# Performance work log

Measured on AMD Instinct MI355X. Metric: run time of the kernel, lower is better.

## Reference

```python
import jax, jax.numpy as jnp
import numpy as np

B, S, E, H = 2, 2048, 2048, 16
D = E // H          # head_dim = 128
RD = 128            # rotary_emb_dim (== head_dim here)
BASE = 10000.0


def setup_inputs() -> dict:
    key = jax.random.key(0)
    k1, k2, k3, k4, k5 = jax.random.split(key, 5)
    scale = 0.02
    return {
        "x": jax.random.normal(k1, (B, S, E), dtype=jnp.float32),
        "wqkv_w": jax.random.normal(k2, (3 * E, E), dtype=jnp.float32) * scale,
        "wqkv_b": jax.random.normal(k3, (3 * E,), dtype=jnp.float32) * scale,
        "out_w": jax.random.normal(k4, (E, E), dtype=jnp.float32) * scale,
        "out_b": jax.random.normal(k5, (E,), dtype=jnp.float32) * scale,
    }


def _rope_cos_sin(seqlen, dtype):
    inv_freq = 1.0 / (BASE ** (jnp.arange(0, RD, 2, dtype=jnp.float32) / RD))
    t = jnp.arange(seqlen, dtype=jnp.float32)
    freqs = jnp.outer(t, inv_freq)          # (S, RD//2)
    return jnp.cos(freqs).astype(dtype), jnp.sin(freqs).astype(dtype)


def _apply_rotary(v, cos, sin):
    # v: (B, S, H, D); rotate first RD dims (here RD == D)
    v_rot, v_pass = v[..., :RD], v[..., RD:]
    v1, v2 = jnp.split(v_rot, 2, axis=-1)    # each (B, S, H, RD//2)
    c = cos[None, :, None, :]
    s = sin[None, :, None, :]
    rot = jnp.concatenate([v1 * c - v2 * s, v1 * s + v2 * c], axis=-1)
    return jnp.concatenate([rot, v_pass], axis=-1)


def reference(x, wqkv_w, wqkv_b, out_w, out_b):
    b, s, e = x.shape
    # column-parallel QKV projection (world size 1)
    qkv = jnp.einsum("bse,fe->bsf", x, wqkv_w) + wqkv_b     # (B, S, 3E)
    qkv = qkv.reshape(b, s, 3, H, D)
    cos, sin = _rope_cos_sin(s, x.dtype)
    q = _apply_rotary(qkv[:, :, 0], cos, sin)               # (B, S, H, D)
    k = _apply_rotary(qkv[:, :, 1], cos, sin)
    v = qkv[:, :, 2]
    # causal self-attention, softmax_scale = 1/sqrt(head_dim)
    scale = 1.0 / jnp.sqrt(jnp.asarray(D, dtype=x.dtype))
    scores = jnp.einsum("bshd,bthd->bhst", q, k) * scale    # (B, H, S, S)
    causal_mask = jnp.tril(jnp.ones((s, s), dtype=bool))
    scores = jnp.where(causal_mask[None, None], scores, jnp.finfo(x.dtype).min)
    probs = jax.nn.softmax(scores, axis=-1)
    ctx = jnp.einsum("bhst,bthd->bshd", probs, v)           # (B, S, H, D)
    # row-parallel output projection
    out = jnp.einsum("bse,fe->bsf", ctx.reshape(b, s, e), out_w) + out_b
    return out
```

## Files before the change

### kernel.cpp

```cpp
#include <hip/hip_runtime.h>
#include <cstdint>
#include <cstddef>

#define Bd 2
#define Sd 2048
#define Ed 2048
#define Hd 16
#define Dd 128
#define N3E 6144
#define ATT_SCALE 0.08838834764831845f

typedef short bf16x8 __attribute__((ext_vector_type(8)));
typedef float f32x4 __attribute__((ext_vector_type(4)));

__device__ __forceinline__ float bf2f(unsigned short u) {
    union { unsigned int u; float f; } c;
    c.u = ((unsigned int)u) << 16;
    return c.f;
}
__device__ __forceinline__ unsigned short f2bf(float f) {
    union { float f; unsigned int u; } c;
    c.f = f;
    unsigned int x = c.u;
    x += 0x7FFFu + ((x >> 16) & 1u);
    return (unsigned short)(x >> 16);
}

__device__ __forceinline__ void gl2lds16(const void* g, void* l) {
    __builtin_amdgcn_global_load_lds(
        (const __attribute__((address_space(1))) void*)g,
        (__attribute__((address_space(3))) void*)l, 16, 0, 0);
}

__global__ void cvt_f32_bf16(const float* __restrict__ src,
                             unsigned short* __restrict__ dst, int n) {
    int i = (blockIdx.x * 256 + threadIdx.x) * 4;
    if (i >= n) return;
    const float4 v = *(const float4*)(src + i);
    dst[i + 0] = f2bf(v.x);
    dst[i + 1] = f2bf(v.y);
    dst[i + 2] = f2bf(v.z);
    dst[i + 3] = f2bf(v.w);
}

template <int MODE>
__global__ void gemm_bt(const unsigned short* __restrict__ A,
                        const unsigned short* __restrict__ Bm,
                        const float* __restrict__ bias,
                        void* __restrict__ o0, void* __restrict__ o1,
                        void* __restrict__ o2, int Ndim, int K) {
    __shared__ __align__(16) unsigned short As[128 * 64];
    __shared__ __align__(16) unsigned short Bs[128 * 64];

    const int tid = threadIdx.x;
    const int lane = tid & 63;
    const int wave = tid >> 6;
    const int quad = lane >> 4;
    const int l16 = lane & 15;
    const int wr = wave >> 1;
    const int wc = wave & 1;

    const int n0 = blockIdx.x * 128;
    const int m0 = blockIdx.y * 128;

    const unsigned short* Ab = A + (size_t)m0 * K;
    const unsigned short* Bb = Bm + (size_t)n0 * K;

    const f32x4 fzero = {0.f, 0.f, 0.f, 0.f};
    f32x4 acc[4][4];
#pragma unroll
    for (int i = 0; i < 4; i++)
#pragma unroll
        for (int j = 0; j < 4; j++) acc[i][j] = fzero;

    for (int k0 = 0; k0 < K; k0 += 64) {
        __syncthreads();
#pragma unroll
        for (int it = 0; it < 4; ++it) {
            int L = it * 256 + tid;
            int row = L >> 3;
            int cs = L & 7;
            int gc = cs ^ (row & 7);
            gl2lds16(Ab + row * K + k0 + gc * 8, (void*)(As + L * 8));
            gl2lds16(Bb + row * K + k0 + gc * 8, (void*)(Bs + L * 8));
        }
        __syncthreads();
#pragma unroll
        for (int kk = 0; kk < 2; ++kk) {
            bf16x8 af[4], bfr[4];
#pragma unroll
            for (int i = 0; i < 4; i++) {
                int row = wr * 64 + i * 16 + l16;
                int cs = kk * 4 + quad;
                af[i] = *(const bf16x8*)(As + row * 64 + (cs ^ (row & 7)) * 8);
            }
#pragma unroll
            for (int j = 0; j < 4; j++) {
                int row = wc * 64 + j * 16 + l16;
                int cs = kk * 4 + quad;
                bfr[j] = *(const bf16x8*)(Bs + row * 64 + (cs ^ (row & 7)) * 8);
            }
#pragma unroll
            for (int i = 0; i < 4; i++)
#pragma unroll
                for (int j = 0; j < 4; j++)
                    acc[i][j] = __builtin_amdgcn_mfma_f32_16x16x32_bf16(
                        af[i], bfr[j], acc[i][j], 0, 0, 0);
        }
    }

#pragma unroll
    for (int j = 0; j < 4; j++) {
        int col = n0 + wc * 64 + j * 16 + l16;
        float bv = bias[col];
#pragma unroll
        for (int i = 0; i < 4; i++) {
            int rbase = m0 + wr * 64 + i * 16 + quad * 4;
#pragma unroll
            for (int r = 0; r < 4; r++) {
                float val = acc[i][j][r] + bv;
                int row = rbase + r;
                if (MODE == 0) {
                    ((float*)o0)[(size_t)row * Ndim + col] = val;
                } else {
                    int b = row >> 11;
                    int s = row & 2047;
                    int c = col >> 11;
                    int h = (col >> 7) & 15;
                    int d = col & 127;
                    unsigned short* dst = (c == 0) ? (unsigned short*)o0
                                        : (c == 1) ? (unsigned short*)o1
                                                   : (unsigned short*)o2;
                    dst[((size_t)(b * Hd + h) * Sd + s) * Dd + d] = f2bf(val);
                }
            }
        }
    }
}

__global__ void rope_qk(unsigned short* __restrict__ q,
                        unsigned short* __restrict__ k) {
    int idx = blockIdx.x * 256 + threadIdx.x;
    const int half = Bd * Hd * Sd * 64;
    unsigned short* p = (idx < half) ? q : k;
    int i = (idx < half) ? idx : idx - half;
    int j = i & 63;
    int s = (i >> 6) & (Sd - 1);
    int bh = i >> 17;
    int base = (bh * Sd + s) * Dd;
    float inv_freq = __expf(-(float)j * (9.210340371976184f / 64.0f));
    float fr = (float)s * inv_freq;
    float sn, cs;
    __sincosf(fr, &sn, &cs);
    float v1 = bf2f(p[base + j]);
    float v2 = bf2f(p[base + j + 64]);
    p[base + j] = f2bf(v1 * cs - v2 * sn);
    p[base + j + 64] = f2bf(v1 * sn + v2 * cs);
}

__global__ void transpose_v(const unsigned short* __restrict__ v,
                            unsigned short* __restrict__ vt) {
    __shared__ unsigned short t[32][33];
    int bh = blockIdx.z;
    int s0 = blockIdx.x * 32;
    int d0 = blockIdx.y * 32;
    int tx = threadIdx.x, ty = threadIdx.y;
    const unsigned short* src = v + ((size_t)bh * Sd + s0) * Dd + d0;
    for (int r = ty; r < 32; r += 8) t[r][tx] = src[(size_t)r * Dd + tx];
    __syncthreads();
    unsigned short* dst = vt + ((size_t)bh * Dd + d0) * Sd + s0;
    for (int r = ty; r < 32; r += 8) dst[(size_t)r * Sd + tx] = t[tx][r];
}

__global__ __launch_bounds__(256, 4) void flash_attn(
    const unsigned short* __restrict__ q, const unsigned short* __restrict__ k,
    const unsigned short* __restrict__ vt, unsigned short* __restrict__ ctx) {
    __shared__ __align__(16) unsigned short Ks[64 * 128];
    __shared__ __align__(16) unsigned short Vts[128 * 64];
    __shared__ __align__(16) unsigned short Ps[64 * 64];

    const int tid = threadIdx.x;
    const int lane = tid & 63;
    const int wave = tid >> 6;
    const int quad = lane >> 4;
    const int l16 = lane & 15;
    const int rw0 = wave * 16;
    const int ql = rw0 + l16;
    const int qsw = ql & 7;

    const int yy = blockIdx.y;
    const int kq = yy >> 3, y0 = yy & 7;
    const int qi = (kq == 0) ? 31 - y0 : (kq == 1) ? y0 : (kq == 2) ? 23 - y0 : 8 + y0;
    const int bh = blockIdx.x;
    const int q0 = qi * 64;

    const unsigned short* qb = q + ((size_t)bh * Sd + q0) * Dd;
    const unsigned short* kb = k + (size_t)bh * Sd * Dd;
    const unsigned short* vtb = vt + (size_t)bh * Dd * Sd;

#pragma unroll
    for (int it = 0; it < 4; ++it) {
        int L = it * 256 + tid;
        int row = L >> 4;
        int cs = L & 15;
        int gc = cs ^ (row & 15);
        gl2lds16(qb + row * Dd + gc * 8, (void*)(Ks + L * 8));
    }
    __syncthreads();
    bf16x8 aq[4];
#pragma unroll
    for (int kk = 0; kk < 4; kk++)
        aq[kk] = *(const bf16x8*)(Ks + ql * 128 + ((kk * 4 + quad) ^ (ql & 15)) * 8);
    __syncthreads();

    const f32x4 fzero = {0.f, 0.f, 0.f, 0.f};
    f32x4 o[8];
#pragma unroll
    for (int jd = 0; jd < 8; jd++) o[jd] = fzero;
    float mi = -3.0e38f, li = 0.f;

    for (int t0 = 0; t0 <= q0; t0 += 64) {
#pragma unroll
        for (int it = 0; it < 4; ++it) {
            int L = it * 256 + tid;
            int rk = L >> 4;
            int ck = L & 15;
            int gk = ck ^ (rk & 15);
            gl2lds16(kb + (size_t)(t0 + rk) * Dd + gk * 8, (void*)(Ks + L * 8));
            int rv = L >> 3;
            int cv = L & 7;
            int gv = cv ^ (rv & 7);
            gl2lds16(vtb + (size_t)rv * Sd + t0 + gv * 8, (void*)(Vts + L * 8));
        }
        __syncthreads();

        f32x4 sa[4];
#pragma unroll
        for (int j = 0; j < 4; j++) sa[j] = fzero;
#pragma unroll
        for (int kk = 0; kk < 4; kk++) {
            bf16x8 bk[4];
#pragma unroll
            for (int j = 0; j < 4; j++) {
                int rowt = j * 16 + l16;
                bk[j] = *(const bf16x8*)(Ks + rowt * 128 +
                                         ((kk * 4 + quad) ^ (rowt & 15)) * 8);
            }
#pragma unroll
            for (int j = 0; j < 4; j++)
                sa[j] = __builtin_amdgcn_mfma_f32_16x16x32_bf16(bk[j], aq[kk],
                                                                sa[j], 0, 0, 0);
        }

#pragma unroll
        for (int j = 0; j < 4; j++)
#pragma unroll
            for (int r = 0; r < 4; r++) sa[j][r] *= ATT_SCALE;
        if (t0 == q0) {
            const int qg = rw0 + l16;
#pragma unroll
            for (int j = 0; j < 4; j++)
#pragma unroll
                for (int r = 0; r < 4; r++)
                    if ((j * 16 + quad * 4 + r) > qg) sa[j][r] = -3.0e38f;
        }

        float mx = -3.0e38f;
#pragma unroll
        for (int j = 0; j < 4; j++)
#pragma unroll
            for (int r = 0; r < 4; r++) mx = fmaxf(mx, sa[j][r]);
        mx = fmaxf(mx, __shfl_xor(mx, 16, 64));
        mx = fmaxf(mx, __shfl_xor(mx, 32, 64));
        const float mnew = fmaxf(mi, mx);
        const float alpha = __expf(mi - mnew);
        float rs = 0.f;
#pragma unroll
        for (int j = 0; j < 4; j++)
#pragma unroll
            for (int r = 0; r < 4; r++) {
                float pp = __expf(sa[j][r] - mnew);
                sa[j][r] = pp;
                rs += pp;
            }
        rs += __shfl_xor(rs, 16, 64);
        rs += __shfl_xor(rs, 32, 64);
        li = li * alpha + rs;
        mi = mnew;

#pragma unroll
        for (int j = 0; j < 4; j++) {
            ushort4 pk;
            pk.x = f2bf(sa[j][0]);
            pk.y = f2bf(sa[j][1]);
            pk.z = f2bf(sa[j][2]);
            pk.w = f2bf(sa[j][3]);
            *(ushort4*)(Ps + ql * 64 + ((j * 2 + (quad >> 1)) ^ qsw) * 8 +
                        (quad & 1) * 4) = pk;
        }

        float av[4];
#pragma unroll
        for (int r = 0; r < 4; r++) av[r] = __shfl(alpha, quad * 4 + r, 64);
#pragma unroll
        for (int jd = 0; jd < 8; jd++)
#pragma unroll
            for (int r = 0; r < 4; r++) o[jd][r] *= av[r];

#pragma unroll
        for (int kk = 0; kk < 2; kk++) {
            bf16x8 ap = *(const bf16x8*)(Ps + ql * 64 +
                                         ((kk * 4 + quad) ^ qsw) * 8);
            bf16x8 bv[8];
#pragma unroll
            for (int jd = 0; jd < 8; jd++) {
                int d = jd * 16 + l16;
                bv[jd] = *(const bf16x8*)(Vts + d * 64 +
                                          ((kk * 4 + quad) ^ (d & 7)) * 8);
            }
#pragma unroll
            for (int jd = 0; jd < 8; jd++)
                o[jd] = __builtin_amdgcn_mfma_f32_16x16x32_bf16(ap, bv[jd],
                                                                o[jd], 0, 0, 0);
        }
        __syncthreads();
    }

    const int b = bh >> 4;
    const int h = bh & 15;
    float linv[4];
#pragma unroll
    for (int r = 0; r < 4; r++) linv[r] = 1.0f / __shfl(li, quad * 4 + r, 64);
#pragma unroll
    for (int r = 0; r < 4; r++) {
        const int grow = q0 + rw0 + quad * 4 + r;
        unsigned short* dst = ctx + ((size_t)(b * Sd + grow)) * Ed + h * Dd;
#pragma unroll
        for (int jd = 0; jd < 8; jd++)
            dst[jd * 16 + l16] = f2bf(o[jd][r] * linv[r]);
    }
}

extern "C" void kernel_launch(void* const* d_in, const int* in_sizes, int n_in,
                              void* d_out, int out_size, void* d_ws,
                              size_t ws_size, hipStream_t stream) {
    const float* x = (const float*)d_in[0];
    const float* wqkv_w = (const float*)d_in[1];
    const float* wqkv_b = (const float*)d_in[2];
    const float* out_w = (const float*)d_in[3];
    const float* out_b = (const float*)d_in[4];
    float* out = (float*)d_out;

    char* ws = (char*)d_ws;
    unsigned short* xb    = (unsigned short*)(ws + 0);
    unsigned short* wqkvb = (unsigned short*)(ws + 16777216);
    unsigned short* owb   = (unsigned short*)(ws + 41943040);
    unsigned short* qb    = (unsigned short*)(ws + 50331648);
    unsigned short* kb    = (unsigned short*)(ws + 67108864);
    unsigned short* vb    = (unsigned short*)(ws + 83886080);
    unsigned short* vtb   = (unsigned short*)(ws + 0);
    unsigned short* ctx   = (unsigned short*)(ws + 16777216);

    cvt_f32_bf16<<<8192, 256, 0, stream>>>(x, xb, 8388608);
    cvt_f32_bf16<<<12288, 256, 0, stream>>>(wqkv_w, wqkvb, 12582912);
    cvt_f32_bf16<<<4096, 256, 0, stream>>>(out_w, owb, 4194304);

    gemm_bt<1><<<dim3(48, 32), 256, 0, stream>>>(xb, wqkvb, wqkv_b, qb, kb, vb,
                                                 N3E, Ed);
    rope_qk<<<32768, 256, 0, stream>>>(qb, kb);
    transpose_v<<<dim3(64, 4, 32), dim3(32, 8), 0, stream>>>(vb, vtb);
    flash_attn<<<dim3(32, 32), 256, 0, stream>>>(qb, kb, vtb, ctx);
    gemm_bt<0><<<dim3(16, 32), 256, 0, stream>>>(ctx, owb, out_b, out, nullptr,
                                                 nullptr, Ed, Ed);
}
```

Measured before the change: 372.6 us.

## Fuse RoPE and V transpose into QKV GEMM epilogue, merge conversions

```diff
diff --git a/kernel.cpp b/kernel.cpp
--- a/kernel.cpp
+++ b/kernel.cpp
@@ -32,15 +32,24 @@
         (__attribute__((address_space(3))) void*)l, 16, 0, 0);
 }
 
-__global__ void cvt_f32_bf16(const float* __restrict__ src,
-                             unsigned short* __restrict__ dst, int n) {
+__global__ void cvt_all(const float* __restrict__ x,
+                        const float* __restrict__ w1,
+                        const float* __restrict__ w2,
+                        unsigned short* __restrict__ ox,
+                        unsigned short* __restrict__ o1,
+                        unsigned short* __restrict__ o2) {
     int i = (blockIdx.x * 256 + threadIdx.x) * 4;
-    if (i >= n) return;
-    const float4 v = *(const float4*)(src + i);
-    dst[i + 0] = f2bf(v.x);
-    dst[i + 1] = f2bf(v.y);
-    dst[i + 2] = f2bf(v.z);
-    dst[i + 3] = f2bf(v.w);
+    const float* s;
+    unsigned short* d;
+    int off;
+    if (i < 8388608) { s = x; d = ox; off = i; }
+    else if (i < 20971520) { s = w1; d = o1; off = i - 8388608; }
+    else { s = w2; d = o2; off = i - 20971520; }
+    const float4 v = *(const float4*)(s + off);
+    d[off + 0] = f2bf(v.x);
+    d[off + 1] = f2bf(v.y);
+    d[off + 2] = f2bf(v.z);
+    d[off + 3] = f2bf(v.w);
 }
 
 template <int MODE>
@@ -49,8 +58,9 @@
                         const float* __restrict__ bias,
                         void* __restrict__ o0, void* __restrict__ o1,
                         void* __restrict__ o2, int Ndim, int K) {
-    __shared__ __align__(16) unsigned short As[128 * 64];
-    __shared__ __align__(16) unsigned short Bs[128 * 64];
+    __shared__ __align__(16) unsigned short U[16640];
+    unsigned short* As = U;
+    unsigned short* Bs = U + 8192;
 
     const int tid = threadIdx.x;
     const int lane = tid & 63;
@@ -109,67 +119,88 @@
         }
     }
 
-#pragma unroll
-    for (int j = 0; j < 4; j++) {
-        int col = n0 + wc * 64 + j * 16 + l16;
-        float bv = bias[col];
-#pragma unroll
-        for (int i = 0; i < 4; i++) {
-            int rbase = m0 + wr * 64 + i * 16 + quad * 4;
-#pragma unroll
-            for (int r = 0; r < 4; r++) {
-                float val = acc[i][j][r] + bv;
-                int row = rbase + r;
-                if (MODE == 0) {
-                    ((float*)o0)[(size_t)row * Ndim + col] = val;
-                } else {
-                    int b = row >> 11;
-                    int s = row & 2047;
-                    int c = col >> 11;
-                    int h = (col >> 7) & 15;
-                    int d = col & 127;
-                    unsigned short* dst = (c == 0) ? (unsigned short*)o0
-                                        : (c == 1) ? (unsigned short*)o1
-                                                   : (unsigned short*)o2;
-                    dst[((size_t)(b * Hd + h) * Sd + s) * Dd + d] = f2bf(val);
-                }
+    if (MODE == 0) {
+#pragma unroll
+        for (int j = 0; j < 4; j++) {
+            int col = n0 + wc * 64 + j * 16 + l16;
+            float bv = bias[col];
+#pragma unroll
+            for (int i = 0; i < 4; i++) {
+                int rbase = m0 + wr * 64 + i * 16 + quad * 4;
+#pragma unroll
+                for (int r = 0; r < 4; r++)
+                    ((float*)o0)[(size_t)(rbase + r) * Ndim + col] =
+                        acc[i][j][r] + bv;
+            }
+        }
+    } else {
+        __syncthreads();
+#pragma unroll
+        for (int j = 0; j < 4; j++) {
+            int coll = wc * 64 + j * 16 + l16;
+            float bv = bias[n0 + coll];
+#pragma unroll
+            for (int i = 0; i < 4; i++) {
+                int rl = wr * 64 + i * 16 + quad * 4;
+#pragma unroll
+                for (int r = 0; r < 4; r++)
+                    U[(rl + r) * 130 + coll] = f2bf(acc[i][j][r] + bv);
+            }
+        }
+        __syncthreads();
+
+        const int ch = n0 >> 7;
+        const int c = ch >> 4;
+        const int h = ch & 15;
+        const int bb = m0 >> 11;
+        const int s0 = m0 & 2047;
+
+        if (c < 2) {
+            unsigned short* dstq = (unsigned short*)(c == 0 ? o0 : o1);
+            const size_t hb = ((size_t)(bb * Hd + h)) * Sd;
+#pragma unroll
+            for (int it = 0; it < 16; ++it) {
+                int lin = it * 256 + tid;
+                int row = lin >> 5, p = lin & 31;
+                int s = s0 + row;
+                unsigned int lo = *(const unsigned int*)(U + row * 130 + 2 * p);
+                unsigned int hi =
+                    *(const unsigned int*)(U + row * 130 + 64 + 2 * p);
+                float v1a = bf2f((unsigned short)lo), v1b = bf2f(lo >> 16);
+                float v2a = bf2f((unsigned short)hi), v2b = bf2f(hi >> 16);
+                float fa = (float)s * __expf(-(float)(2 * p) *
+                                             (9.210340371976184f / 64.0f));
+                float fb = (float)s * __expf(-(float)(2 * p + 1) *
+                                             (9.210340371976184f / 64.0f));
+                float sna, csa, snb, csb;
+                __sincosf(fa, &sna, &csa);
+                __sincosf(fb, &snb, &csb);
+                ushort2 r1, r2;
+                r1.x = f2bf(v1a * csa - v2a * sna);
+                r1.y = f2bf(v1b * csb - v2b * snb);
+                r2.x = f2bf(v1a * sna + v2a * csa);
+                r2.y = f2bf(v1b * snb + v2b * csb);
+                unsigned short* dst = dstq + (hb + s) * Dd;
+                *(ushort2*)(dst + 2 * p) = r1;
+                *(ushort2*)(dst + 64 + 2 * p) = r2;
+            }
+        } else {
+            unsigned short* dstv = (unsigned short*)o2;
+            const size_t hb = ((size_t)(bb * Hd + h)) * Dd;
+#pragma unroll
+            for (int it = 0; it < 16; ++it) {
+                int lin = it * 256 + tid;
+                int d = lin >> 5, sc = lin & 31;
+                int s4 = sc * 4;
+                ushort4 pk;
+                pk.x = U[(s4 + 0) * 130 + d];
+                pk.y = U[(s4 + 1) * 130 + d];
+                pk.z = U[(s4 + 2) * 130 + d];
+                pk.w = U[(s4 + 3) * 130 + d];
+                *(ushort4*)(dstv + (hb + d) * Sd + s0 + s4) = pk;
             }
         }
     }
-}
-
-__global__ void rope_qk(unsigned short* __restrict__ q,
-                        unsigned short* __restrict__ k) {
-    int idx = blockIdx.x * 256 + threadIdx.x;
-    const int half = Bd * Hd * Sd * 64;
-    unsigned short* p = (idx < half) ? q : k;
-    int i = (idx < half) ? idx : idx - half;
-    int j = i & 63;
-    int s = (i >> 6) & (Sd - 1);
-    int bh = i >> 17;
-    int base = (bh * Sd + s) * Dd;
-    float inv_freq = __expf(-(float)j * (9.210340371976184f / 64.0f));
-    float fr = (float)s * inv_freq;
-    float sn, cs;
-    __sincosf(fr, &sn, &cs);
-    float v1 = bf2f(p[base + j]);
-    float v2 = bf2f(p[base + j + 64]);
-    p[base + j] = f2bf(v1 * cs - v2 * sn);
-    p[base + j + 64] = f2bf(v1 * sn + v2 * cs);
-}
-
-__global__ void transpose_v(const unsigned short* __restrict__ v,
-                            unsigned short* __restrict__ vt) {
-    __shared__ unsigned short t[32][33];
-    int bh = blockIdx.z;
-    int s0 = blockIdx.x * 32;
-    int d0 = blockIdx.y * 32;
-    int tx = threadIdx.x, ty = threadIdx.y;
-    const unsigned short* src = v + ((size_t)bh * Sd + s0) * Dd + d0;
-    for (int r = ty; r < 32; r += 8) t[r][tx] = src[(size_t)r * Dd + tx];
-    __syncthreads();
-    unsigned short* dst = vt + ((size_t)bh * Dd + d0) * Sd + s0;
-    for (int r = ty; r < 32; r += 8) dst[(size_t)r * Sd + tx] = t[tx][r];
 }
 
 __global__ __launch_bounds__(256, 4) void flash_attn(
@@ -357,18 +388,12 @@
     unsigned short* owb   = (unsigned short*)(ws + 41943040);
     unsigned short* qb    = (unsigned short*)(ws + 50331648);
     unsigned short* kb    = (unsigned short*)(ws + 67108864);
-    unsigned short* vb    = (unsigned short*)(ws + 83886080);
-    unsigned short* vtb   = (unsigned short*)(ws + 0);
-    unsigned short* ctx   = (unsigned short*)(ws + 16777216);
-
-    cvt_f32_bf16<<<8192, 256, 0, stream>>>(x, xb, 8388608);
-    cvt_f32_bf16<<<12288, 256, 0, stream>>>(wqkv_w, wqkvb, 12582912);
-    cvt_f32_bf16<<<4096, 256, 0, stream>>>(out_w, owb, 4194304);
-
-    gemm_bt<1><<<dim3(48, 32), 256, 0, stream>>>(xb, wqkvb, wqkv_b, qb, kb, vb,
+    unsigned short* vtb   = (unsigned short*)(ws + 83886080);
+    unsigned short* ctx   = (unsigned short*)(ws + 0);
+
+    cvt_all<<<24576, 256, 0, stream>>>(x, wqkv_w, out_w, xb, wqkvb, owb);
+    gemm_bt<1><<<dim3(48, 32), 256, 0, stream>>>(xb, wqkvb, wqkv_b, qb, kb, vtb,
                                                  N3E, Ed);
-    rope_qk<<<32768, 256, 0, stream>>>(qb, kb);
-    transpose_v<<<dim3(64, 4, 32), dim3(32, 8), 0, stream>>>(vb, vtb);
     flash_attn<<<dim3(32, 32), 256, 0, stream>>>(qb, kb, vtb, ctx);
     gemm_bt<0><<<dim3(16, 32), 256, 0, stream>>>(ctx, owb, out_b, out, nullptr,
                                                  nullptr, Ed, Ed);
```

New measurement: 350.8 us. -5.9%, faster.
